# Performance work log

Hardware: AMD Instinct MI355X
Metric: run time of the kernel (lower is better)

Reference implementation:

```python
import jax, jax.numpy as jnp
import numpy as np

N_MAX = 20
REG_WEIGHT = 0.01


def setup_inputs() -> dict:
    key = jax.random.key(0)
    k1, k2, k3, k4 = jax.random.split(key, 4)
    target = jax.random.normal(k1, (32, 512, 2048), dtype=jnp.float32)
    pred = jax.random.normal(k2, (32, 512, 2048), dtype=jnp.float32)
    latent = jax.random.normal(k3, (64800,), dtype=jnp.float32)
    # R_xyz: xyz coordinates of each field point (buffer from get_field()), shape [3, G]
    R_xyz = jax.random.normal(k4, (3, 64800), dtype=jnp.float32)
    return {"target": target, "pred": pred, "latent": latent, "R_xyz": R_xyz}


def reference(target, pred, latent, R_xyz):
    # L1 loss (mean reduction)
    l1 = jnp.mean(jnp.abs(target - pred))

    # Regularizer: std of pairwise distances of the xyz positions of the
    # top-N_max latent activations.
    _, idx = jax.lax.top_k(latent, N_MAX)          # [N_max] int indices
    max_xyz = R_xyz[:, idx].T                       # [N_max, 3]

    # F.pdist(p=2): upper-triangle (i<j) pairwise Euclidean distances
    iu, ju = jnp.triu_indices(N_MAX, k=1)
    diff = max_xyz[iu] - max_xyz[ju]                # [N_max*(N_max-1)/2, 3]
    dists = jnp.sqrt(jnp.sum(diff * diff, axis=-1))

    # torch.std defaults to unbiased (ddof=1)
    reg = jnp.std(dists, ddof=1)

    total = l1 + REG_WEIGHT * reg
    return (total, l1, REG_WEIGHT * reg)
```

## Files before the change

### kernel.cpp

```cpp
#include <hip/hip_runtime.h>
#include <hip/hip_bf16.h>

#define NMAX 20
#define NPAIR (NMAX * (NMAX - 1) / 2)
#define TPB 256
#define L1_BLOCKS 2048
#define TOPK_BLOCKS 16
#define UNROLL 8

__device__ __forceinline__ unsigned long long packKey(float v, unsigned i) {
    unsigned u = __float_as_uint(v);
    u = (u & 0x80000000u) ? ~u : (u | 0x80000000u);
    return ((unsigned long long)u << 32) | (unsigned long long)(~i);
}

__device__ __forceinline__ float absdiff4(float4 a, float4 b) {
    return fabsf(a.x - b.x) + fabsf(a.y - b.y) +
           fabsf(a.z - b.z) + fabsf(a.w - b.w);
}

__global__ void __launch_bounds__(TPB, 4)
fused_kernel(const float4* __restrict__ t, const float4* __restrict__ p, int nvec,
             const float* __restrict__ latent, int nLat,
             float* __restrict__ partial, unsigned long long* __restrict__ keysOut) {
    if (blockIdx.x >= TOPK_BLOCKS) {
        int bid = blockIdx.x - TOPK_BLOCKS;
        int stride = L1_BLOCKS * TPB;
        int i = bid * TPB + threadIdx.x;

        float acc[UNROLL];
        #pragma unroll
        for (int k = 0; k < UNROLL; ++k) acc[k] = 0.f;

        while (i + (UNROLL - 1) * stride < nvec) {
            float4 a[UNROLL], b[UNROLL];
            #pragma unroll
            for (int k = 0; k < UNROLL; ++k) a[k] = t[i + k * stride];
            #pragma unroll
            for (int k = 0; k < UNROLL; ++k) b[k] = p[i + k * stride];
            #pragma unroll
            for (int k = 0; k < UNROLL; ++k) acc[k] += absdiff4(a[k], b[k]);
            i += UNROLL * stride;
        }
        for (; i < nvec; i += stride) acc[0] += absdiff4(t[i], p[i]);

        float s = 0.f;
        #pragma unroll
        for (int k = 0; k < UNROLL; ++k) s += acc[k];

        #pragma unroll
        for (int o = 32; o > 0; o >>= 1) s += __shfl_down(s, o, 64);
        __shared__ float wsum[TPB / 64];
        int lane = threadIdx.x & 63;
        int wid  = threadIdx.x >> 6;
        if (lane == 0) wsum[wid] = s;
        __syncthreads();
        if (threadIdx.x == 0) {
            float tot = 0.f;
            #pragma unroll
            for (int w = 0; w < TPB / 64; ++w) tot += wsum[w];
            partial[bid] = tot;
        }
    } else {
        int b   = blockIdx.x;
        int tid = threadIdx.x;
        int lane = tid & 63, wid = tid >> 6;

        unsigned long long loc[NMAX];
        #pragma unroll
        for (int k = 0; k < NMAX; ++k) loc[k] = 0ull;

        for (int i = b * TPB + tid; i < nLat; i += TOPK_BLOCKS * TPB) {
            unsigned long long key = packKey(latent[i], (unsigned)i);
            #pragma unroll
            for (int k = NMAX - 1; k >= 1; --k) {
                loc[k] = (key > loc[k - 1]) ? loc[k - 1]
                                            : ((key > loc[k]) ? key : loc[k]);
            }
            loc[0] = (key > loc[0]) ? key : loc[0];
        }

        __shared__ unsigned long long wmax[TPB / 64];
        __shared__ unsigned long long selk;
        unsigned long long prev = ~0ull;
        for (int r = 0; r < NMAX; ++r) {
            unsigned long long m = 0ull;
            #pragma unroll
            for (int k = 0; k < NMAX; ++k) {
                unsigned long long c = loc[k];
                m = (c < prev && c > m) ? c : m;
            }
            #pragma unroll
            for (int o = 32; o > 0; o >>= 1) {
                unsigned long long other = __shfl_down(m, o, 64);
                if (other > m) m = other;
            }
            if (lane == 0) wmax[wid] = m;
            __syncthreads();
            if (tid == 0) {
                unsigned long long mm = wmax[0];
                #pragma unroll
                for (int w = 1; w < TPB / 64; ++w) if (wmax[w] > mm) mm = wmax[w];
                selk = mm;
                keysOut[b * NMAX + r] = mm;
            }
            __syncthreads();
            prev = selk;
        }
    }
}

__global__ void __launch_bounds__(TPB)
finalize_kernel(const float* __restrict__ partials, int nPartials,
                const unsigned long long* __restrict__ keys,
                const float* __restrict__ R_xyz, int G,
                float* __restrict__ out, float invN) {
    __shared__ float red[TPB];
    __shared__ unsigned long long ck[TOPK_BLOCKS * NMAX];
    __shared__ unsigned long long wmax[TPB / 64];
    __shared__ unsigned long long selk;
    __shared__ int   sel[NMAX];
    __shared__ float sxyz[NMAX][3];
    __shared__ float s_l1, s_sum;

    int tid = threadIdx.x, lane = tid & 63, wid = tid >> 6;

    {
        float s = 0.f;
        for (int i = tid; i < nPartials; i += TPB) s += partials[i];
        red[tid] = s;
        __syncthreads();
        for (int off = TPB / 2; off > 0; off >>= 1) {
            if (tid < off) red[tid] += red[tid + off];
            __syncthreads();
        }
        if (tid == 0) s_l1 = red[0] * invN;
        __syncthreads();
    }

    for (int i = tid; i < TOPK_BLOCKS * NMAX; i += TPB) ck[i] = keys[i];
    __syncthreads();
    {
        unsigned long long prev = ~0ull;
        for (int r = 0; r < NMAX; ++r) {
            unsigned long long m = 0ull;
            for (int i = tid; i < TOPK_BLOCKS * NMAX; i += TPB) {
                unsigned long long c = ck[i];
                m = (c < prev && c > m) ? c : m;
            }
            #pragma unroll
            for (int o = 32; o > 0; o >>= 1) {
                unsigned long long other = __shfl_down(m, o, 64);
                if (other > m) m = other;
            }
            if (lane == 0) wmax[wid] = m;
            __syncthreads();
            if (tid == 0) {
                unsigned long long mm = wmax[0];
                #pragma unroll
                for (int w = 1; w < TPB / 64; ++w) if (wmax[w] > mm) mm = wmax[w];
                selk = mm;
                sel[r] = (int)(~(unsigned)mm);
            }
            __syncthreads();
            prev = selk;
        }
    }

    if (tid < NMAX * 3) {
        int i = tid / 3, d = tid % 3;
        sxyz[i][d] = R_xyz[d * G + sel[i]];
    }
    __syncthreads();

    float dval = 0.f;
    if (tid < NPAIR) {
        int k = tid, i = 0, rem = NMAX - 1;
        while (k >= rem) { k -= rem; ++i; --rem; }
        int j = i + 1 + k;
        float dx = sxyz[i][0] - sxyz[j][0];
        float dy = sxyz[i][1] - sxyz[j][1];
        float dz = sxyz[i][2] - sxyz[j][2];
        dval = sqrtf(dx * dx + dy * dy + dz * dz);
    }
    red[tid] = dval;
    __syncthreads();
    for (int off = TPB / 2; off > 0; off >>= 1) {
        if (tid < off) red[tid] += red[tid + off];
        __syncthreads();
    }
    if (tid == 0) s_sum = red[0];
    __syncthreads();
    red[tid] = dval * dval;
    __syncthreads();
    for (int off = TPB / 2; off > 0; off >>= 1) {
        if (tid < off) red[tid] += red[tid + off];
        __syncthreads();
    }
    if (tid == 0) {
        float sum   = s_sum;
        float sumsq = red[0];
        float mean  = sum / (float)NPAIR;
        float var   = (sumsq - (float)NPAIR * mean * mean) / (float)(NPAIR - 1);
        float stdv  = sqrtf(fmaxf(var, 0.f));
        float reg   = 0.01f * stdv;
        out[0] = s_l1 + reg;
        out[1] = s_l1;
        out[2] = reg;
    }
}

extern "C" void kernel_launch(void* const* d_in, const int* in_sizes, int n_in,
                              void* d_out, int out_size, void* d_ws, size_t ws_size,
                              hipStream_t stream) {
    const float* target = (const float*)d_in[0];
    const float* pred   = (const float*)d_in[1];
    const float* latent = (const float*)d_in[2];
    const float* R_xyz  = (const float*)d_in[3];
    float* out = (float*)d_out;

    int n    = in_sizes[0];
    int nLat = in_sizes[2];
    int G    = in_sizes[3] / 3;
    int nvec = n / 4;

    float* partials = (float*)d_ws;
    unsigned long long* keys = (unsigned long long*)((char*)d_ws + L1_BLOCKS * sizeof(float));

    fused_kernel<<<TOPK_BLOCKS + L1_BLOCKS, TPB, 0, stream>>>(
        (const float4*)target, (const float4*)pred, nvec,
        latent, nLat, partials, keys);

    finalize_kernel<<<1, TPB, 0, stream>>>(
        partials, L1_BLOCKS, keys, R_xyz, G, out, 1.0f / (float)n);
}
```

Before: 71.90 us.

## Fuse finalize into main kernel via last-block atomic counter, use nontemporal loads

Merges the separate finalize kernel into the main kernel. Each block increments a global counter after writing its partial, and the last block to arrive performs the final reduction, top-k merge and std computation. L1 loads become nontemporal, and the total block count is capped at 2048, so the L1 path gets 16 fewer blocks. This removes one kernel launch and its gap, but adds a memset launch plus threadfence/atomic overhead.

```diff
diff --git a/kernel.cpp b/kernel.cpp
--- a/kernel.cpp
+++ b/kernel.cpp
@@ -4,9 +4,12 @@
 #define NMAX 20
 #define NPAIR (NMAX * (NMAX - 1) / 2)
 #define TPB 256
-#define L1_BLOCKS 2048
 #define TOPK_BLOCKS 16
+#define TOTAL_BLOCKS 2048
+#define L1_BLOCKS (TOTAL_BLOCKS - TOPK_BLOCKS)
 #define UNROLL 8
+
+typedef float f4 __attribute__((ext_vector_type(4)));
 
 __device__ __forceinline__ unsigned long long packKey(float v, unsigned i) {
     unsigned u = __float_as_uint(v);
@@ -14,107 +17,17 @@
     return ((unsigned long long)u << 32) | (unsigned long long)(~i);
 }
 
-__device__ __forceinline__ float absdiff4(float4 a, float4 b) {
+__device__ __forceinline__ float absdiff4(f4 a, f4 b) {
     return fabsf(a.x - b.x) + fabsf(a.y - b.y) +
            fabsf(a.z - b.z) + fabsf(a.w - b.w);
 }
 
 __global__ void __launch_bounds__(TPB, 4)
-fused_kernel(const float4* __restrict__ t, const float4* __restrict__ p, int nvec,
-             const float* __restrict__ latent, int nLat,
-             float* __restrict__ partial, unsigned long long* __restrict__ keysOut) {
-    if (blockIdx.x >= TOPK_BLOCKS) {
-        int bid = blockIdx.x - TOPK_BLOCKS;
-        int stride = L1_BLOCKS * TPB;
-        int i = bid * TPB + threadIdx.x;
-
-        float acc[UNROLL];
-        #pragma unroll
-        for (int k = 0; k < UNROLL; ++k) acc[k] = 0.f;
-
-        while (i + (UNROLL - 1) * stride < nvec) {
-            float4 a[UNROLL], b[UNROLL];
-            #pragma unroll
-            for (int k = 0; k < UNROLL; ++k) a[k] = t[i + k * stride];
-            #pragma unroll
-            for (int k = 0; k < UNROLL; ++k) b[k] = p[i + k * stride];
-            #pragma unroll
-            for (int k = 0; k < UNROLL; ++k) acc[k] += absdiff4(a[k], b[k]);
-            i += UNROLL * stride;
-        }
-        for (; i < nvec; i += stride) acc[0] += absdiff4(t[i], p[i]);
-
-        float s = 0.f;
-        #pragma unroll
-        for (int k = 0; k < UNROLL; ++k) s += acc[k];
-
-        #pragma unroll
-        for (int o = 32; o > 0; o >>= 1) s += __shfl_down(s, o, 64);
-        __shared__ float wsum[TPB / 64];
-        int lane = threadIdx.x & 63;
-        int wid  = threadIdx.x >> 6;
-        if (lane == 0) wsum[wid] = s;
-        __syncthreads();
-        if (threadIdx.x == 0) {
-            float tot = 0.f;
-            #pragma unroll
-            for (int w = 0; w < TPB / 64; ++w) tot += wsum[w];
-            partial[bid] = tot;
-        }
-    } else {
-        int b   = blockIdx.x;
-        int tid = threadIdx.x;
-        int lane = tid & 63, wid = tid >> 6;
-
-        unsigned long long loc[NMAX];
-        #pragma unroll
-        for (int k = 0; k < NMAX; ++k) loc[k] = 0ull;
-
-        for (int i = b * TPB + tid; i < nLat; i += TOPK_BLOCKS * TPB) {
-            unsigned long long key = packKey(latent[i], (unsigned)i);
-            #pragma unroll
-            for (int k = NMAX - 1; k >= 1; --k) {
-                loc[k] = (key > loc[k - 1]) ? loc[k - 1]
-                                            : ((key > loc[k]) ? key : loc[k]);
-            }
-            loc[0] = (key > loc[0]) ? key : loc[0];
-        }
-
-        __shared__ unsigned long long wmax[TPB / 64];
-        __shared__ unsigned long long selk;
-        unsigned long long prev = ~0ull;
-        for (int r = 0; r < NMAX; ++r) {
-            unsigned long long m = 0ull;
-            #pragma unroll
-            for (int k = 0; k < NMAX; ++k) {
-                unsigned long long c = loc[k];
-                m = (c < prev && c > m) ? c : m;
-            }
-            #pragma unroll
-            for (int o = 32; o > 0; o >>= 1) {
-                unsigned long long other = __shfl_down(m, o, 64);
-                if (other > m) m = other;
-            }
-            if (lane == 0) wmax[wid] = m;
-            __syncthreads();
-            if (tid == 0) {
-                unsigned long long mm = wmax[0];
-                #pragma unroll
-                for (int w = 1; w < TPB / 64; ++w) if (wmax[w] > mm) mm = wmax[w];
-                selk = mm;
-                keysOut[b * NMAX + r] = mm;
-            }
-            __syncthreads();
-            prev = selk;
-        }
-    }
-}
-
-__global__ void __launch_bounds__(TPB)
-finalize_kernel(const float* __restrict__ partials, int nPartials,
-                const unsigned long long* __restrict__ keys,
-                const float* __restrict__ R_xyz, int G,
-                float* __restrict__ out, float invN) {
+fused_all(const f4* __restrict__ t, const f4* __restrict__ p, int nvec,
+          const float* __restrict__ latent, int nLat,
+          const float* __restrict__ R_xyz, int G,
+          float* __restrict__ partial, unsigned long long* __restrict__ keysOut,
+          unsigned int* __restrict__ counter, float* __restrict__ out, float invN) {
     __shared__ float red[TPB];
     __shared__ unsigned long long ck[TOPK_BLOCKS * NMAX];
     __shared__ unsigned long long wmax[TPB / 64];
@@ -122,12 +35,104 @@
     __shared__ int   sel[NMAX];
     __shared__ float sxyz[NMAX][3];
     __shared__ float s_l1, s_sum;
+    __shared__ int   s_last;
 
     int tid = threadIdx.x, lane = tid & 63, wid = tid >> 6;
+
+    if (blockIdx.x >= TOPK_BLOCKS) {
+        int bid = blockIdx.x - TOPK_BLOCKS;
+        int stride = L1_BLOCKS * TPB;
+        int i = bid * TPB + tid;
+
+        float acc[UNROLL];
+        #pragma unroll
+        for (int k = 0; k < UNROLL; ++k) acc[k] = 0.f;
+
+        while (i + (UNROLL - 1) * stride < nvec) {
+            f4 a[UNROLL], b[UNROLL];
+            #pragma unroll
+            for (int k = 0; k < UNROLL; ++k) a[k] = __builtin_nontemporal_load(&t[i + k * stride]);
+            #pragma unroll
+            for (int k = 0; k < UNROLL; ++k) b[k] = __builtin_nontemporal_load(&p[i + k * stride]);
+            #pragma unroll
+            for (int k = 0; k < UNROLL; ++k) acc[k] += absdiff4(a[k], b[k]);
+            i += UNROLL * stride;
+        }
+        for (; i < nvec; i += stride)
+            acc[0] += absdiff4(__builtin_nontemporal_load(&t[i]),
+                               __builtin_nontemporal_load(&p[i]));
+
+        float s = 0.f;
+        #pragma unroll
+        for (int k = 0; k < UNROLL; ++k) s += acc[k];
+
+        #pragma unroll
+        for (int o = 32; o > 0; o >>= 1) s += __shfl_down(s, o, 64);
+        if (lane == 0) red[wid] = s;
+        __syncthreads();
+        if (tid == 0) {
+            float tot = 0.f;
+            #pragma unroll
+            for (int w = 0; w < TPB / 64; ++w) tot += red[w];
+            partial[bid] = tot;
+        }
+    } else {
+        int b = blockIdx.x;
+
+        unsigned long long loc[NMAX];
+        #pragma unroll
+        for (int k = 0; k < NMAX; ++k) loc[k] = 0ull;
+
+        for (int i = b * TPB + tid; i < nLat; i += TOPK_BLOCKS * TPB) {
+            unsigned long long key = packKey(latent[i], (unsigned)i);
+            #pragma unroll
+            for (int k = NMAX - 1; k >= 1; --k) {
+                loc[k] = (key > loc[k - 1]) ? loc[k - 1]
+                                            : ((key > loc[k]) ? key : loc[k]);
+            }
+            loc[0] = (key > loc[0]) ? key : loc[0];
+        }
+
+        unsigned long long prev = ~0ull;
+        for (int r = 0; r < NMAX; ++r) {
+            unsigned long long m = 0ull;
+            #pragma unroll
+            for (int k = 0; k < NMAX; ++k) {
+                unsigned long long c = loc[k];
+                m = (c < prev && c > m) ? c : m;
+            }
+            #pragma unroll
+            for (int o = 32; o > 0; o >>= 1) {
+                unsigned long long other = __shfl_down(m, o, 64);
+                if (other > m) m = other;
+            }
+            if (lane == 0) wmax[wid] = m;
+            __syncthreads();
+            if (tid == 0) {
+                unsigned long long mm = wmax[0];
+                #pragma unroll
+                for (int w = 1; w < TPB / 64; ++w) if (wmax[w] > mm) mm = wmax[w];
+                selk = mm;
+                keysOut[b * NMAX + r] = mm;
+            }
+            __syncthreads();
+            prev = selk;
+        }
+    }
+
+    __syncthreads();
+    if (tid == 0) {
+        __threadfence();
+        unsigned int prevc = atomicAdd(counter, 1u);
+        s_last = (prevc == TOTAL_BLOCKS - 1) ? 1 : 0;
+    }
+    __syncthreads();
+    if (!s_last) return;
+    __threadfence();
 
     {
         float s = 0.f;
-        for (int i = tid; i < nPartials; i += TPB) s += partials[i];
+        for (int i = tid; i < L1_BLOCKS; i += TPB) s += partial[i];
         red[tid] = s;
         __syncthreads();
         for (int off = TPB / 2; off > 0; off >>= 1) {
@@ -138,7 +143,7 @@
         __syncthreads();
     }
 
-    for (int i = tid; i < TOPK_BLOCKS * NMAX; i += TPB) ck[i] = keys[i];
+    for (int i = tid; i < TOPK_BLOCKS * NMAX; i += TPB) ck[i] = keysOut[i];
     __syncthreads();
     {
         unsigned long long prev = ~0ull;
@@ -224,13 +229,13 @@
     int G    = in_sizes[3] / 3;
     int nvec = n / 4;
 
-    float* partials = (float*)d_ws;
-    unsigned long long* keys = (unsigned long long*)((char*)d_ws + L1_BLOCKS * sizeof(float));
-
-    fused_kernel<<<TOPK_BLOCKS + L1_BLOCKS, TPB, 0, stream>>>(
-        (const float4*)target, (const float4*)pred, nvec,
-        latent, nLat, partials, keys);
-
-    finalize_kernel<<<1, TPB, 0, stream>>>(
-        partials, L1_BLOCKS, keys, R_xyz, G, out, 1.0f / (float)n);
-}
+    unsigned int* counter = (unsigned int*)d_ws;
+    float* partials = (float*)((char*)d_ws + 64);
+    unsigned long long* keys = (unsigned long long*)((char*)d_ws + 64 + 8192);
+
+    (void)hipMemsetAsync(counter, 0, sizeof(unsigned int), stream);
+
+    fused_all<<<TOTAL_BLOCKS, TPB, 0, stream>>>(
+        (const f4*)target, (const f4*)pred, nvec,
+        latent, nLat, R_xyz, G, partials, keys, counter, out, 1.0f / (float)n);
+}
```

New measurement: 165.1 us. +129.6%, slower.
